# Optimization experiments

Measured on AMD Instinct MI355X. Metric: run time of the kernel, lower is better.

The kernel has to match this reference:

```python
import jax, jax.numpy as jnp
import numpy as np

Bsz, Hs, Ws, D = 16, 48, 48, 768
N, R, NITERS = 64, 4, 12
NR = N * R


def setup_inputs() -> dict:
    key = jax.random.key(0)
    ks = jax.random.split(key, 16)
    w = lambda k, shape, s=0.02: jax.random.normal(k, shape, jnp.float32) * s
    return {
        "x": jax.random.normal(ks[0], (Bsz, Hs, Ws, D), jnp.float32),
        "W_B": w(ks[1], (D, NR)), "b_B": jnp.zeros((NR,), jnp.float32),
        "W_C": w(ks[2], (D, NR)), "b_C": jnp.zeros((NR,), jnp.float32),
        "W_X": w(ks[3], (D, R)), "b_X": jnp.zeros((R,), jnp.float32),
        "W_dec": w(ks[4], (D, N)), "b_dec": jnp.zeros((N,), jnp.float32),
        "W_th": w(ks[5], (D, N // 2)), "b_th": jnp.zeros((N // 2,), jnp.float32),
        "W_lam": w(ks[6], (D, 1)), "b_lam": jnp.zeros((1,), jnp.float32),
        "B_bias": jnp.ones((NR,), jnp.float32),
        "C_bias": jnp.ones((NR,), jnp.float32),
        "conv_w": w(ks[7], (3, 3, 1, N), 0.1),  # HWIO, depthwise (groups=N)
        "conv_b": jnp.zeros((N,), jnp.float32),
        "W_out": w(ks[8], (NR, D)), "b_out": jnp.zeros((D,), jnp.float32),
    }


def _rope(v, th):
    # v: [B,R,H,W,N], th: [B,H,W,N/2] (broadcast over R). Interleaved pairs.
    c = jnp.cos(th)[:, None]
    s = jnp.sin(th)[:, None]
    vr = v.reshape(v.shape[:-1] + (v.shape[-1] // 2, 2))
    v1, v2 = vr[..., 0], vr[..., 1]
    return jnp.stack([v1 * c - v2 * s, v1 * s + v2 * c], axis=-1).reshape(v.shape)


def reference(x, W_B, b_B, W_C, b_C, W_X, b_X, W_dec, b_dec, W_th, b_th,
              W_lam, b_lam, B_bias, C_bias, conv_w, conv_b, W_out, b_out):
    silu = jax.nn.silu
    Bb, Hh, Ww = x.shape[0], x.shape[1], x.shape[2]

    # Input-dependent (iteration-invariant) projections
    B_proj = silu(x @ W_B + b_B + B_bias).reshape(Bb, Hh, Ww, N, R)
    C_proj = silu(x @ W_C + b_C + C_bias).reshape(Bb, Hh, Ww, N, R)
    B_base = jnp.transpose(B_proj, (0, 4, 1, 2, 3))  # [B,R,H,W,N]
    C_base = jnp.transpose(C_proj, (0, 4, 1, 2, 3))
    Xb = jnp.transpose(silu(x @ W_X + b_X), (0, 3, 1, 2))[..., None]  # [B,R,H,W,1]
    alpha = jax.nn.sigmoid(x @ W_dec + b_dec)[:, None]  # [B,1,H,W,N]
    theta = x @ W_th + b_th                              # [B,H,W,N/2]
    gamma = jax.nn.sigmoid(x @ W_lam + b_lam)[:, None]  # [B,1,H,W,1]

    def diffuse(Hst):
        hf = Hst.reshape(Bb * R, Hh, Ww, N)
        y = jax.lax.conv_general_dilated(
            hf, conv_w, (1, 1), 'SAME',
            dimension_numbers=('NHWC', 'HWIO', 'NHWC'),
            feature_group_count=N) + conv_b
        return y.reshape(Bb, R, Hh, Ww, N)

    Hst = jnp.zeros((Bb, R, Hh, Ww, N), x.dtype)
    prev = None
    for i in range(NITERS):
        inj = _rope(B_base, theta * (i + 1)) * Xb
        Hst = diffuse(Hst)
        if prev is None:
            Hst = alpha * Hst + inj
        else:
            Hst = alpha * Hst + (1.0 - gamma) * alpha * prev + gamma * inj
        prev = inj

    C_rot = _rope(C_base, theta * NITERS)  # layer_idx = n_iters-1 -> scale n_iters
    Hg = C_rot * Hst                        # [B,R,H,W,N]
    Ho = jnp.transpose(Hg, (0, 2, 3, 1, 4)).reshape(Bb, Hh, Ww, R * N)
    return silu(Ho @ W_out + b_out)
```

## Files before the change

kernel.cpp:

```cpp
#include <hip/hip_runtime.h>
#include <hip/hip_bf16.h>
#include <math.h>

#define PTOT 36864
#define DIM 768
#define NCOLS 640
#define IMG 2304
#define KSTEPS 24
#define NPBLK 288

typedef unsigned short ushort_t;
typedef unsigned int uint_t;
typedef __attribute__((ext_vector_type(8))) short bfx8;
typedef __attribute__((ext_vector_type(4))) float f32x4;

#define MFMA_BF16(a, b, c) __builtin_amdgcn_mfma_f32_16x16x32_bf16((a), (b), (c), 0, 0, 0)

__device__ __forceinline__ float sigmoidf_(float v) { return 1.f / (1.f + __expf(-v)); }
__device__ __forceinline__ float siluf_(float v)    { return v   / (1.f + __expf(-v)); }
__device__ __forceinline__ float rfl(float v) {
  return __int_as_float(__builtin_amdgcn_readfirstlane(__float_as_int(v)));
}
__device__ __forceinline__ float bf2f(ushort_t h) {
  return __uint_as_float(((uint_t)h) << 16);
}

typedef __attribute__((address_space(3))) unsigned int lds_uint;
typedef __attribute__((address_space(1))) const unsigned int g_uint;
__device__ __forceinline__ void glds16(const void* gsrc, void* ldst) {
  __builtin_amdgcn_global_load_lds((g_uint*)gsrc, (lds_uint*)ldst, 16, 0, 0);
}

__device__ __forceinline__ void split2(float a, float b, uint_t& hw, uint_t& lw) {
  __hip_bfloat162 hh = __float22bfloat162_rn(make_float2(a, b));
  uint_t hu; __builtin_memcpy(&hu, &hh, 4);
  float ha = __uint_as_float(hu << 16);
  float hb = __uint_as_float(hu & 0xffff0000u);
  __hip_bfloat162 ll = __float22bfloat162_rn(make_float2(a - ha, b - hb));
  uint_t lu; __builtin_memcpy(&lu, &ll, 4);
  hw = hu; lw = lu;
}
__device__ __forceinline__ uint_t cvt2_hi(float a, float b) {
  __hip_bfloat162 hh = __float22bfloat162_rn(make_float2(a, b));
  uint_t hu; __builtin_memcpy(&hu, &hh, 4);
  return hu;
}
__device__ __forceinline__ ushort_t f2bf(float a) {
  return (ushort_t)(cvt2_hi(a, 0.f) & 0xffffu);
}
__device__ __forceinline__ void split8_fast(const float* f, uint4& hi, uint4& lo) {
  uint_t* Hp = (uint_t*)&hi;
  uint_t* Lp = (uint_t*)&lo;
#pragma unroll
  for (int q = 0; q < 4; ++q) split2(f[2 * q], f[2 * q + 1], Hp[q], Lp[q]);
}
__device__ __forceinline__ void cvt8_hi(const float* f, uint4& hi) {
  uint_t* Hp = (uint_t*)&hi;
#pragma unroll
  for (int q = 0; q < 4; ++q) Hp[q] = cvt2_hi(f[2 * q], f[2 * q + 1]);
}

__global__ void pack_kernel(
    const float* __restrict__ W_B, const float* __restrict__ W_C,
    const float* __restrict__ W_dec, const float* __restrict__ W_th,
    const float* __restrict__ W_X, const float* __restrict__ W_lam,
    const float* __restrict__ b_B, const float* __restrict__ b_C,
    const float* __restrict__ b_dec, const float* __restrict__ b_th,
    const float* __restrict__ b_X, const float* __restrict__ b_lam,
    const float* __restrict__ B_bias, const float* __restrict__ C_bias,
    const float* __restrict__ W_out,
    ushort_t* __restrict__ WhiT, ushort_t* __restrict__ WloT,
    ushort_t* __restrict__ WoT, float* __restrict__ bias_all) {
  int idx = blockIdx.x * 256 + threadIdx.x;
  const int NW = NCOLS * DIM;
  const int NWO = DIM * 256;
  if (idx < NW) {
    int c = idx / DIM, k = idx - c * DIM;
    float v;
    if      (c < 256) v = W_B[k * 256 + c];
    else if (c < 512) v = W_C[k * 256 + (c - 256)];
    else if (c < 576) v = W_dec[k * 64 + (c - 512)];
    else if (c < 608) v = W_th[k * 32 + (c - 576)];
    else if (c < 612) v = W_X[k * 4 + (c - 608)];
    else if (c == 612) v = W_lam[k];
    else v = 0.f;
    uint_t hw, lw;
    split2(v, 0.f, hw, lw);
    WhiT[idx] = (ushort_t)(hw & 0xffffu);
    WloT[idx] = (ushort_t)(lw & 0xffffu);
  } else if (idx < NW + NWO) {
    int t = idx - NW;
    int j = t / 256, k = t - j * 256;
    WoT[t] = f2bf(W_out[k * DIM + j]);
  }
  if (idx < NCOLS) {
    int c = idx;
    float v;
    if      (c < 256) v = b_B[c] + B_bias[c];
    else if (c < 512) v = b_C[c - 256] + C_bias[c - 256];
    else if (c < 576) v = b_dec[c - 512];
    else if (c < 608) v = b_th[c - 576];
    else if (c < 612) v = b_X[c - 608];
    else if (c == 612) v = b_lam[0];
    else v = 0.f;
    bias_all[c] = v;
  }
}

__global__ __launch_bounds__(512, 4) void gemm_proj_fused(
    const float* __restrict__ x, const ushort_t* __restrict__ WhiT,
    const ushort_t* __restrict__ WloT, const float* __restrict__ biasall,
    ushort_t* __restrict__ projBC, float* __restrict__ projS) {
  __shared__ ushort_t S[2][16384];
  const int tid = threadIdx.x;
  const int lane = tid & 63, wv = tid >> 6;
  const int wr = wv >> 2, wc = wv & 3;
  const int lk = lane >> 4, lm = lane & 15;

  f32x4 acc[4][2];
#pragma unroll
  for (int i = 0; i < 4; ++i)
#pragma unroll
    for (int j = 0; j < 2; ++j) acc[i][j] = (f32x4)0.f;

  if (blockIdx.x < 1152) {
    int lin = blockIdx.x;
    int id2 = (lin & 7) * 144 + (lin >> 3);
    const int cblk = id2 & 3, pblk = id2 >> 2;
    const int c0 = cblk * 128, p0 = pblk * 128;

    const int r0 = tid >> 3,         s0 = tid & 7,         g0 = s0 ^ (r0 & 7);
    const int r1 = (tid + 512) >> 3, s1 = (tid + 512) & 7, g1 = s1 ^ (r1 & 7);
    const float* xsrc0 = x + (size_t)(p0 + r0) * DIM + g0 * 8;
    const float* xsrc1 = x + (size_t)(p0 + r1) * DIM + g1 * 8;

    float4 xr[4];

    auto stageW = [&](int buf, int ph) {
      const int k0 = ph * 64;
#pragma unroll
      for (int j = 0; j < 2; ++j) {
        int mb = __builtin_amdgcn_readfirstlane(j * 512 + wv * 64);
        int m = mb + lane;
        int row = m >> 3, sp = m & 7;
        int g = sp ^ (row & 7);
        glds16(&WhiT[(size_t)(c0 + row) * DIM + k0 + g * 8],
               (void*)&S[buf][mb * 8]);
      }
    };
    auto loadX = [&](int ph) {
      const float* q0 = xsrc0 + ph * 64;
      xr[0] = *(const float4*)q0;
      xr[1] = *(const float4*)(q0 + 4);
      const float* q1 = xsrc1 + ph * 64;
      xr[2] = *(const float4*)q1;
      xr[3] = *(const float4*)(q1 + 4);
    };
    auto writeX = [&](int buf) {
      float fv[8];
      uint4 hv;
      *(float4*)&fv[0] = xr[0]; *(float4*)&fv[4] = xr[1];
      cvt8_hi(fv, hv);
      *(uint4*)&S[buf][8192 + (size_t)tid * 8] = hv;
      *(float4*)&fv[0] = xr[2]; *(float4*)&fv[4] = xr[3];
      cvt8_hi(fv, hv);
      *(uint4*)&S[buf][8192 + (size_t)(tid + 512) * 8] = hv;
    };

    loadX(0);
    stageW(0, 0);
    writeX(0);

    for (int ph = 0; ph < 12; ++ph) {
      const int cur = ph & 1;
      __syncthreads();
      if (ph + 1 < 12) {
        loadX(ph + 1);
        stageW(cur ^ 1, ph + 1);
      }
#pragma unroll
      for (int s = 0; s < 2; ++s) {
        bfx8 ah[4];
#pragma unroll
        for (int f = 0; f < 4; ++f) {
          int row = wr * 64 + f * 16 + lm;
          int slot = (s * 4 + lk) ^ (row & 7);
          ah[f] = *(const bfx8*)&S[cur][(row * 8 + slot) * 8];
        }
        bfx8 bh[2];
#pragma unroll
        for (int n = 0; n < 2; ++n) {
          int row = wc * 32 + n * 16 + lm;
          int slot = (s * 4 + lk) ^ (row & 7);
          bh[n] = *(const bfx8*)&S[cur][8192 + (row * 8 + slot) * 8];
        }
#pragma unroll
        for (int i = 0; i < 4; ++i)
#pragma unroll
          for (int j = 0; j < 2; ++j)
            acc[i][j] = MFMA_BF16(ah[i], bh[j], acc[i][j]);
      }
      if (ph + 1 < 12) writeX(cur ^ 1);
    }

#pragma unroll
    for (int i = 0; i < 4; ++i) {
#pragma unroll
      for (int r = 0; r < 4; ++r) {
        int c = c0 + wr * 64 + i * 16 + lk * 4 + r;
        float bia = biasall[c];
#pragma unroll
        for (int j = 0; j < 2; ++j) {
          float z = siluf_(acc[i][j][r] + bia);
          projBC[(size_t)c * PTOT + p0 + wc * 32 + j * 16 + lm] = f2bf(z);
        }
      }
    }
  } else {
    int lin = blockIdx.x - 1152;
    int id2 = (lin & 7) * 36 + (lin >> 3);
    const int pblk = id2;
    const int c0 = 512, p0 = pblk * 128;

    auto stage = [&](int buf, int kidx) {
      const int k0 = kidx * 32;
      {
        int mb = __builtin_amdgcn_readfirstlane(wv * 64);
        int m = mb + lane;
        int row = m >> 2, sp = m & 3;
        int g = sp ^ ((row >> 1) & 3);
        glds16(&WhiT[(size_t)(c0 + row) * DIM + k0 + g * 8],
               (void*)&S[buf][mb * 8]);
      }
      {
        int mb = __builtin_amdgcn_readfirstlane(wv * 64);
        int m = mb + lane;
        int row = m >> 2, sp = m & 3;
        int g = sp ^ ((row >> 1) & 3);
        glds16(&WloT[(size_t)(c0 + row) * DIM + k0 + g * 8],
               (void*)&S[buf][4096 + mb * 8]);
      }
      float* Xf = (float*)&S[buf][8192];
#pragma unroll
      for (int j = 0; j < 2; ++j) {
        int mb = __builtin_amdgcn_readfirstlane(j * 512 + wv * 64);
        int m = mb + lane;
        int row = m >> 3, sp = m & 7;
        int g = sp ^ (row & 7);
        glds16(&x[(size_t)(p0 + row) * DIM + k0 + g * 4],
               (void*)&Xf[mb * 4]);
      }
    };

    stage(0, 0);
    __syncthreads();

    for (int kidx = 0; kidx < KSTEPS; ++kidx) {
      const int cur = kidx & 1;
      if (kidx + 1 < KSTEPS) stage(cur ^ 1, kidx + 1);

      bfx8 ah[4], al[4];
#pragma unroll
      for (int f = 0; f < 4; ++f) {
        int row = wr * 64 + f * 16 + lm;
        int sp = lk ^ ((row >> 1) & 3);
        int idx = (row * 4 + sp) * 8;
        ah[f] = *(const bfx8*)&S[cur][idx];
        al[f] = *(const bfx8*)&S[cur][4096 + idx];
      }
      const float* Xf = (const float*)&S[cur][8192];
      bfx8 bh[2], bl[2];
#pragma unroll
      for (int n = 0; n < 2; ++n) {
        int row = wc * 32 + n * 16 + lm;
        int sp0 = (2 * lk)     ^ (row & 7);
        int sp1 = (2 * lk + 1) ^ (row & 7);
        float fv[8];
        *(float4*)&fv[0] = *(const float4*)&Xf[(row * 8 + sp0) * 4];
        *(float4*)&fv[4] = *(const float4*)&Xf[(row * 8 + sp1) * 4];
        uint4 hv, lv;
        split8_fast(fv, hv, lv);
        bh[n] = *(bfx8*)&hv;
        bl[n] = *(bfx8*)&lv;
      }
#pragma unroll
      for (int i = 0; i < 4; ++i)
#pragma unroll
        for (int j = 0; j < 2; ++j) {
          acc[i][j] = MFMA_BF16(ah[i], bh[j], acc[i][j]);
          acc[i][j] = MFMA_BF16(al[i], bh[j], acc[i][j]);
          acc[i][j] = MFMA_BF16(ah[i], bl[j], acc[i][j]);
        }
      __syncthreads();
    }

#pragma unroll
    for (int i = 0; i < 4; ++i) {
#pragma unroll
      for (int r = 0; r < 4; ++r) {
        int c = c0 + wr * 64 + i * 16 + lk * 4 + r;
        if (c >= 613) continue;
        float bia = biasall[c];
        int rowo = c - 512;
        bool do_silu = (c >= 608 && c < 612);
        bool do_sig  = (c < 576) || (c == 612);
#pragma unroll
        for (int j = 0; j < 2; ++j) {
          float z = acc[i][j][r] + bia;
          if (do_silu) z = siluf_(z);
          else if (do_sig) z = sigmoidf_(z);
          projS[(size_t)rowo * PTOT + p0 + wc * 32 + j * 16 + lm] = z;
        }
      }
    }
  }
}

__global__ __launch_bounds__(256) void iter_kernel(
    const ushort_t* __restrict__ projBC, const float* __restrict__ projS,
    const float* __restrict__ conv_w, const float* __restrict__ conv_b,
    ushort_t* __restrict__ HgBf) {
  const int n2 = blockIdx.x;
  const int r  = blockIdx.y;
  const int b  = blockIdx.z;
  const int n0 = 2 * n2, n1 = n0 + 1;
  const int tid = threadIdx.x;
  const int bh = tid >> 4, bw = tid & 15;
  const int pbase = b * IMG;

  __shared__ float2 HS[2][50 * 51];

  float w0[9], w1[9];
#pragma unroll
  for (int t = 0; t < 9; ++t) {
    w0[t] = rfl(conv_w[t * 64 + n0]);
    w1[t] = rfl(conv_w[t * 64 + n1]);
  }
  const float cvb0 = rfl(conv_b[n0]), cvb1 = rfl(conv_b[n1]);

  {
    float4 zz = {0.f, 0.f, 0.f, 0.f};
    float4* z = (float4*)&HS[0][0];
#pragma unroll
    for (int u = 0; u < 10; ++u) {
      int q = tid + 256 * u;
      if (q < 2550) z[q] = zz;
    }
  }

  const ushort_t* rowB0 = projBC + (size_t)(n0 * 4 + r) * PTOT + pbase;
  const ushort_t* rowB1 = projBC + (size_t)(n1 * 4 + r) * PTOT + pbase;
  const ushort_t* rowC0 = projBC + (size_t)(256 + n0 * 4 + r) * PTOT + pbase;
  const ushort_t* rowC1 = projBC + (size_t)(256 + n1 * 4 + r) * PTOT + pbase;
  const float* rowA0 = projS + (size_t)n0 * PTOT + pbase;
  const float* rowA1 = projS + (size_t)n1 * PTOT + pbase;
  const float* rowTh = projS + (size_t)(64 + n2) * PTOT + pbase;
  const float* rowXv = projS + (size_t)(96 + r) * PTOT + pbase;
  const float* rowGm = projS + (size_t)100 * PTOT + pbase;

  float be0[9], be1[9], cb[9], sb[9], al0[9], al1[9], gmv[9];
#pragma unroll
  for (int s = 0; s < 9; ++s) {
    int dy = s / 3, dx = s - 3 * dy;
    int i = (3 * bh + dy) * 48 + 3 * bw + dx;
    float sn, cn;
    __sincosf(rowTh[i], &sn, &cn);
    cb[s] = cn; sb[s] = sn;
    float B0 = bf2f(rowB0[i]), B1 = bf2f(rowB1[i]), X = rowXv[i];
    be0[s] = (B0 * cn - B1 * sn) * X;
    be1[s] = (B0 * sn + B1 * cn) * X;
    al0[s] = rowA0[i]; al1[s] = rowA1[i];
    gmv[s] = rowGm[i];
  }
  __syncthreads();

  int cur = 0;
  for (int it = 0; it < 12; ++it) {
    float a0[9], a1[9];
#pragma unroll
    for (int s = 0; s < 9; ++s) { a0[s] = cvb0; a1[s] = cvb1; }
#pragma unroll
    for (int yy = 0; yy < 5; ++yy) {
      float2 row[5];
#pragma unroll
      for (int xx = 0; xx < 5; ++xx)
        row[xx] = HS[cur][(3 * bh + yy) * 51 + 3 * bw + xx];
#pragma unroll
      for (int dy = 0; dy < 3; ++dy) {
        int ty = yy - dy;
        if (ty < 0 || ty > 2) continue;
#pragma unroll
        for (int dx = 0; dx < 3; ++dx)
#pragma unroll
          for (int tx = 0; tx < 3; ++tx) {
            a0[dy * 3 + dx] += row[dx + tx].x * w0[ty * 3 + tx];
            a1[dy * 3 + dx] += row[dx + tx].y * w1[ty * 3 + tx];
          }
      }
    }
#pragma unroll
    for (int s = 0; s < 9; ++s) {
      int dy = s / 3, dx = s - 3 * dy;
      float h0, h1;
      if (it == 0) {
        h0 = al0[s] * a0[s] + be0[s];
        h1 = al1[s] * a1[s] + be1[s];
      } else {
        float p0 = be0[s] * cb[s] + be1[s] * sb[s];
        float p1 = be1[s] * cb[s] - be0[s] * sb[s];
        float g = gmv[s];
        h0 = al0[s] * (a0[s] + (1.f - g) * p0) + g * be0[s];
        h1 = al1[s] * (a1[s] + (1.f - g) * p1) + g * be1[s];
      }
      float2 hw; hw.x = h0; hw.y = h1;
      HS[cur ^ 1][(3 * bh + dy + 1) * 51 + (3 * bw + dx + 1)] = hw;
      if (it < 11) {
        float nb0 = be0[s] * cb[s] - be1[s] * sb[s];
        float nb1 = be0[s] * sb[s] + be1[s] * cb[s];
        be0[s] = nb0; be1[s] = nb1;
      }
    }
    __syncthreads();
    cur ^= 1;
  }

  ushort_t* outRow0 = HgBf + (size_t)(r * 64 + n0) * PTOT + pbase;
  ushort_t* outRow1 = HgBf + (size_t)(r * 64 + n1) * PTOT + pbase;
#pragma unroll
  for (int s = 0; s < 9; ++s) {
    int dy = s / 3, dx = s - 3 * dy;
    int i = (3 * bh + dy) * 48 + 3 * bw + dx;
    float c2 = cb[s] * cb[s] - sb[s] * sb[s], s2 = 2.f * cb[s] * sb[s];
    float c4 = c2 * c2 - s2 * s2,             s4 = 2.f * c2 * s2;
    float c8 = c4 * c4 - s4 * s4,             s8 = 2.f * c4 * s4;
    float c12 = c8 * c4 - s8 * s4,            s12 = c8 * s4 + s8 * c4;
    float C0 = bf2f(rowC0[i]), C1 = bf2f(rowC1[i]);
    float cr0 = C0 * c12 - C1 * s12;
    float cr1 = C0 * s12 + C1 * c12;
    float2 hv = HS[cur][(3 * bh + dy + 1) * 51 + (3 * bw + dx + 1)];
    outRow0[i] = f2bf(cr0 * hv.x);
    outRow1[i] = f2bf(cr1 * hv.y);
  }
}

__global__ __launch_bounds__(256) void transpose_cvt(
    const ushort_t* __restrict__ HgBf, ushort_t* __restrict__ Hbf) {
  __shared__ float T[64][65];
  const int tid = threadIdx.x;
  const int p0 = blockIdx.x * 64;
  const int k0 = blockIdx.y * 64;
  {
    int row = tid >> 2, q = tid & 3;
    const ushort_t* src = &HgBf[(size_t)(k0 + row) * PTOT + p0 + q * 16];
    uint4 u0 = *(const uint4*)src;
    uint4 u1 = *(const uint4*)(src + 8);
    const uint_t* up = (const uint_t*)&u0;
#pragma unroll
    for (int t = 0; t < 4; ++t) {
      T[row][q * 16 + 2 * t]     = bf2f((ushort_t)(up[t] & 0xffffu));
      T[row][q * 16 + 2 * t + 1] = bf2f((ushort_t)(up[t] >> 16));
    }
    const uint_t* vp = (const uint_t*)&u1;
#pragma unroll
    for (int t = 0; t < 4; ++t) {
      T[row][q * 16 + 8 + 2 * t]     = bf2f((ushort_t)(vp[t] & 0xffffu));
      T[row][q * 16 + 8 + 2 * t + 1] = bf2f((ushort_t)(vp[t] >> 16));
    }
  }
  __syncthreads();
  {
    int pr = tid >> 2, kq = tid & 3;
    uint_t Hw[8];
#pragma unroll
    for (int q = 0; q < 8; ++q)
      Hw[q] = cvt2_hi(T[kq * 16 + 2 * q][pr], T[kq * 16 + 2 * q + 1][pr]);
    size_t off = (size_t)(p0 + pr) * 256 + k0 + kq * 16;
    *(uint4*)&Hbf[off]     = make_uint4(Hw[0], Hw[1], Hw[2], Hw[3]);
    *(uint4*)&Hbf[off + 8] = make_uint4(Hw[4], Hw[5], Hw[6], Hw[7]);
  }
}

__global__ __launch_bounds__(512, 4) void gemm_out_glds(
    const ushort_t* __restrict__ Hbf, const ushort_t* __restrict__ WoT,
    const float* __restrict__ b_out, float* __restrict__ out) {
  __shared__ ushort_t As[2][8192];
  __shared__ ushort_t Bs[2][8192];
  const int tid = threadIdx.x;
  const int lane = tid & 63, wv = tid >> 6;
  const int wr = wv >> 2, wc = wv & 3;
  const int lk = lane >> 4, lm = lane & 15;
  int lin = blockIdx.x;
  int id2 = (lin & 7) * 216 + (lin >> 3);
  const int jblk = id2 % 6, pblk = id2 / 6;
  const int j0 = jblk * 128, p0 = pblk * 128;

  f32x4 acc[4][2];
#pragma unroll
  for (int i = 0; i < 4; ++i)
#pragma unroll
    for (int j = 0; j < 2; ++j) acc[i][j] = (f32x4)0.f;

  auto stage = [&](int buf, int ph) {
    const int k0 = ph * 64;
#pragma unroll
    for (int j = 0; j < 2; ++j) {
      int mb = __builtin_amdgcn_readfirstlane(j * 512 + wv * 64);
      int m = mb + lane;
      int row = m >> 3, sp = m & 7;
      int g = sp ^ (row & 7);
      glds16(&Hbf[(size_t)(p0 + row) * 256 + k0 + g * 8],
             (void*)&As[buf][mb * 8]);
    }
#pragma unroll
    for (int j = 0; j < 2; ++j) {
      int mb = __builtin_amdgcn_readfirstlane(j * 512 + wv * 64);
      int m = mb + lane;
      int row = m >> 3, sp = m & 7;
      int g = sp ^ (row & 7);
      glds16(&WoT[(size_t)(j0 + row) * 256 + k0 + g * 8],
             (void*)&Bs[buf][mb * 8]);
    }
  };

  stage(0, 0);
  __syncthreads();

  for (int ph = 0; ph < 4; ++ph) {
    const int cur = ph & 1;
    if (ph + 1 < 4) stage(cur ^ 1, ph + 1);
#pragma unroll
    for (int s = 0; s < 2; ++s) {
      bfx8 ah[4], bh[2];
#pragma unroll
      for (int f = 0; f < 4; ++f) {
        int ra = wr * 64 + f * 16 + lm;
        int slot = (s * 4 + lk) ^ (ra & 7);
        ah[f] = *(const bfx8*)&As[cur][(ra * 8 + slot) * 8];
      }
#pragma unroll
      for (int n = 0; n < 2; ++n) {
        int rb = wc * 32 + n * 16 + lm;
        int slot = (s * 4 + lk) ^ (rb & 7);
        bh[n] = *(const bfx8*)&Bs[cur][(rb * 8 + slot) * 8];
      }
#pragma unroll
      for (int i = 0; i < 4; ++i)
#pragma unroll
        for (int j = 0; j < 2; ++j)
          acc[i][j] = MFMA_BF16(ah[i], bh[j], acc[i][j]);
    }
    __syncthreads();
  }

  float bo[2];
#pragma unroll
  for (int jj = 0; jj < 2; ++jj) bo[jj] = b_out[j0 + wc * 32 + jj * 16 + lm];
#pragma unroll
  for (int i = 0; i < 4; ++i) {
#pragma unroll
    for (int r = 0; r < 4; ++r) {
      int p = p0 + wr * 64 + i * 16 + lk * 4 + r;
      size_t rowoff = (size_t)p * DIM;
#pragma unroll
      for (int jj = 0; jj < 2; ++jj) {
        out[rowoff + j0 + wc * 32 + jj * 16 + lm] =
            siluf_(acc[i][jj][r] + bo[jj]);
      }
    }
  }
}

extern "C" void kernel_launch(void* const* d_in, const int* in_sizes, int n_in,
                              void* d_out, int out_size, void* d_ws, size_t ws_size,
                              hipStream_t stream) {
  const float* x      = (const float*)d_in[0];
  const float* W_B    = (const float*)d_in[1];
  const float* b_B    = (const float*)d_in[2];
  const float* W_C    = (const float*)d_in[3];
  const float* b_C    = (const float*)d_in[4];
  const float* W_X    = (const float*)d_in[5];
  const float* b_X    = (const float*)d_in[6];
  const float* W_dec  = (const float*)d_in[7];
  const float* b_dec  = (const float*)d_in[8];
  const float* W_th   = (const float*)d_in[9];
  const float* b_th   = (const float*)d_in[10];
  const float* W_lam  = (const float*)d_in[11];
  const float* b_lam  = (const float*)d_in[12];
  const float* B_bias = (const float*)d_in[13];
  const float* C_bias = (const float*)d_in[14];
  const float* conv_w = (const float*)d_in[15];
  const float* conv_b = (const float*)d_in[16];
  const float* W_out  = (const float*)d_in[17];
  const float* b_out  = (const float*)d_in[18];
  float* out = (float*)d_out;

  ushort_t* WhiT   = (ushort_t*)d_ws;
  ushort_t* WloT   = WhiT + (size_t)NCOLS * DIM;
  ushort_t* WoT    = WloT + (size_t)NCOLS * DIM;
  float* bias_all  = (float*)(WoT + (size_t)DIM * 256);
  ushort_t* projBC = (ushort_t*)(bias_all + NCOLS);
  float* projS     = (float*)(projBC + (size_t)512 * PTOT);
  ushort_t* HgBf   = (ushort_t*)(projS + (size_t)104 * PTOT);
  ushort_t* Hbf    = HgBf + (size_t)256 * PTOT;

  const int pack_elems = NCOLS * DIM + DIM * 256;
  pack_kernel<<<(pack_elems + 255) / 256, 256, 0, stream>>>(
      W_B, W_C, W_dec, W_th, W_X, W_lam,
      b_B, b_C, b_dec, b_th, b_X, b_lam, B_bias, C_bias, W_out,
      WhiT, WloT, WoT, bias_all);

  gemm_proj_fused<<<dim3(1440), 512, 0, stream>>>(
      x, WhiT, WloT, bias_all, projBC, projS);

  iter_kernel<<<dim3(32, 4, 16), 256, 0, stream>>>(
      projBC, projS, conv_w, conv_b, HgBf);

  transpose_cvt<<<dim3(PTOT / 64, 4), 256, 0, stream>>>(HgBf, Hbf);

  gemm_out_glds<<<dim3(6 * NPBLK), 512, 0, stream>>>(
      Hbf, WoT, b_out, out);
}
```

Baseline: 217.9 us.

## Triple-buffer W tiles and deepen X prefetch in projection GEMM

The bf16 projection GEMM path now uses three LDS buffers for the weight tile and two for the converted x tile. Weight loads are issued two phases ahead and x register loads one phase further ahead. The per-phase __syncthreads is replaced by an explicit lgkmcnt(0) wait plus barrier at the end of each phase, with a scheduling fence. LDS grows from 64KB to 80KB per block, which may cut occupancy under the (512,4) launch bounds.

```diff
diff --git a/kernel.cpp b/kernel.cpp
--- a/kernel.cpp
+++ b/kernel.cpp
@@ -15,6 +15,12 @@
 typedef __attribute__((ext_vector_type(4))) float f32x4;
 
 #define MFMA_BF16(a, b, c) __builtin_amdgcn_mfma_f32_16x16x32_bf16((a), (b), (c), 0, 0, 0)
+
+#define LGKM_BARRIER() do {                               \
+    asm volatile("s_waitcnt lgkmcnt(0)" ::: "memory");    \
+    __builtin_amdgcn_s_barrier();                         \
+    __builtin_amdgcn_sched_barrier(0);                    \
+  } while (0)
 
 __device__ __forceinline__ float sigmoidf_(float v) { return 1.f / (1.f + __expf(-v)); }
 __device__ __forceinline__ float siluf_(float v)    { return v   / (1.f + __expf(-v)); }
@@ -111,7 +117,7 @@
     const float* __restrict__ x, const ushort_t* __restrict__ WhiT,
     const ushort_t* __restrict__ WloT, const float* __restrict__ biasall,
     ushort_t* __restrict__ projBC, float* __restrict__ projS) {
-  __shared__ ushort_t S[2][16384];
+  __shared__ ushort_t S[40960];
   const int tid = threadIdx.x;
   const int lane = tid & 63, wv = tid >> 6;
   const int wr = wv >> 2, wc = wv & 3;
@@ -136,7 +142,7 @@
 
     float4 xr[4];
 
-    auto stageW = [&](int buf, int ph) {
+    auto stageW = [&](int wb, int ph) {
       const int k0 = ph * 64;
 #pragma unroll
       for (int j = 0; j < 2; ++j) {
@@ -145,7 +151,7 @@
         int row = m >> 3, sp = m & 7;
         int g = sp ^ (row & 7);
         glds16(&WhiT[(size_t)(c0 + row) * DIM + k0 + g * 8],
-               (void*)&S[buf][mb * 8]);
+               (void*)&S[wb * 8192 + mb * 8]);
       }
     };
     auto loadX = [&](int ph) {
@@ -156,28 +162,29 @@
       xr[2] = *(const float4*)q1;
       xr[3] = *(const float4*)(q1 + 4);
     };
-    auto writeX = [&](int buf) {
+    auto writeX = [&](int xb) {
       float fv[8];
       uint4 hv;
       *(float4*)&fv[0] = xr[0]; *(float4*)&fv[4] = xr[1];
       cvt8_hi(fv, hv);
-      *(uint4*)&S[buf][8192 + (size_t)tid * 8] = hv;
+      *(uint4*)&S[24576 + xb * 8192 + (size_t)tid * 8] = hv;
       *(float4*)&fv[0] = xr[2]; *(float4*)&fv[4] = xr[3];
       cvt8_hi(fv, hv);
-      *(uint4*)&S[buf][8192 + (size_t)(tid + 512) * 8] = hv;
+      *(uint4*)&S[24576 + xb * 8192 + (size_t)(tid + 512) * 8] = hv;
     };
 
+    stageW(0, 0);
     loadX(0);
-    stageW(0, 0);
+    stageW(1, 1);
     writeX(0);
+    loadX(1);
+    LGKM_BARRIER();
 
     for (int ph = 0; ph < 12; ++ph) {
-      const int cur = ph & 1;
-      __syncthreads();
-      if (ph + 1 < 12) {
-        loadX(ph + 1);
-        stageW(cur ^ 1, ph + 1);
-      }
+      const int wb = ph % 3, xb = ph & 1;
+      if (ph + 2 < 12) stageW((ph + 2) % 3, ph + 2);
+      if (ph + 1 < 12) writeX(xb ^ 1);
+      if (ph + 2 < 12) loadX(ph + 2);
 #pragma unroll
       for (int s = 0; s < 2; ++s) {
         bfx8 ah[4];
@@ -185,14 +192,14 @@
         for (int f = 0; f < 4; ++f) {
           int row = wr * 64 + f * 16 + lm;
           int slot = (s * 4 + lk) ^ (row & 7);
-          ah[f] = *(const bfx8*)&S[cur][(row * 8 + slot) * 8];
+          ah[f] = *(const bfx8*)&S[wb * 8192 + (row * 8 + slot) * 8];
         }
         bfx8 bh[2];
 #pragma unroll
         for (int n = 0; n < 2; ++n) {
           int row = wc * 32 + n * 16 + lm;
           int slot = (s * 4 + lk) ^ (row & 7);
-          bh[n] = *(const bfx8*)&S[cur][8192 + (row * 8 + slot) * 8];
+          bh[n] = *(const bfx8*)&S[24576 + xb * 8192 + (row * 8 + slot) * 8];
         }
 #pragma unroll
         for (int i = 0; i < 4; ++i)
@@ -200,7 +207,7 @@
           for (int j = 0; j < 2; ++j)
             acc[i][j] = MFMA_BF16(ah[i], bh[j], acc[i][j]);
       }
-      if (ph + 1 < 12) writeX(cur ^ 1);
+      LGKM_BARRIER();
     }
 
 #pragma unroll
@@ -230,7 +237,7 @@
         int row = m >> 2, sp = m & 3;
         int g = sp ^ ((row >> 1) & 3);
         glds16(&WhiT[(size_t)(c0 + row) * DIM + k0 + g * 8],
-               (void*)&S[buf][mb * 8]);
+               (void*)&S[buf * 16384 + mb * 8]);
       }
       {
         int mb = __builtin_amdgcn_readfirstlane(wv * 64);
@@ -238,9 +245,9 @@
         int row = m >> 2, sp = m & 3;
         int g = sp ^ ((row >> 1) & 3);
         glds16(&WloT[(size_t)(c0 + row) * DIM + k0 + g * 8],
-               (void*)&S[buf][4096 + mb * 8]);
-      }
-      float* Xf = (float*)&S[buf][8192];
+               (void*)&S[buf * 16384 + 4096 + mb * 8]);
+      }
+      float* Xf = (float*)&S[buf * 16384 + 8192];
 #pragma unroll
       for (int j = 0; j < 2; ++j) {
         int mb = __builtin_amdgcn_readfirstlane(j * 512 + wv * 64);
@@ -265,10 +272,10 @@
         int row = wr * 64 + f * 16 + lm;
         int sp = lk ^ ((row >> 1) & 3);
         int idx = (row * 4 + sp) * 8;
-        ah[f] = *(const bfx8*)&S[cur][idx];
-        al[f] = *(const bfx8*)&S[cur][4096 + idx];
-      }
-      const float* Xf = (const float*)&S[cur][8192];
+        ah[f] = *(const bfx8*)&S[cur * 16384 + idx];
+        al[f] = *(const bfx8*)&S[cur * 16384 + 4096 + idx];
+      }
+      const float* Xf = (const float*)&S[cur * 16384 + 8192];
       bfx8 bh[2], bl[2];
 #pragma unroll
       for (int n = 0; n < 2; ++n) {
```

New measurement: 214.8 us (median of 2 runs). Within noise of the previous version (-1.4%).
